# Optimization experiments

Hardware: AMD Instinct MI355X
Metric: run time of the kernel (lower is better)

## Reference

```python
import jax, jax.numpy as jnp
import numpy as np

N_HEAD, BS, F_IN, F_OUT = 4, 8192, 64, 64
LEAKY_ALPHA = 0.2


def setup_inputs() -> dict:
    key = jax.random.key(0)
    k1, k2, k3, k4 = jax.random.split(key, 4)
    return {
        "h": jax.random.normal(k1, (BS, F_IN), dtype=jnp.float32),
        "w": jax.random.normal(k2, (N_HEAD, F_IN, F_OUT), dtype=jnp.float32) * (1.0 / np.sqrt(F_IN)),
        "a_src": jax.random.normal(k3, (N_HEAD, F_OUT, 1), dtype=jnp.float32) * (1.0 / np.sqrt(F_OUT)),
        "a_dst": jax.random.normal(k4, (N_HEAD, F_OUT, 1), dtype=jnp.float32) * (1.0 / np.sqrt(F_OUT)),
        "bias": jnp.zeros((F_OUT,), dtype=jnp.float32),
    }


def reference(h, w, a_src, a_dst, bias):
    # h: [bs, f_in] broadcast-matmul with w: [n_head, f_in, f_out] -> [n_head, bs, f_out]
    h_prime = jnp.einsum("bi,hio->hbo", h, w)
    attn_src = jnp.einsum("hbo,ho->hb", h_prime, a_src[..., 0])  # [n_head, bs]
    attn_dst = jnp.einsum("hbo,ho->hb", h_prime, a_dst[..., 0])  # [n_head, bs]
    # additive scores: [n_head, bs, bs]
    attn = attn_src[:, :, None] + attn_dst[:, None, :]
    attn = jnp.where(attn >= 0, attn, LEAKY_ALPHA * attn)  # leaky_relu(0.2)
    attn = jax.nn.softmax(attn, axis=-1)
    # dropout is identity at inference
    out = jnp.einsum("hbn,hno->hbo", attn, h_prime) + bias  # [n_head, bs, f_out]
    out = jnp.transpose(out, (1, 0, 2))  # [bs, n_head, f_out]
    return out.reshape(out.shape[0], -1)  # [bs, n_head*f_out]
```

## Files before the change

kernel.cpp:

```cpp
#include <hip/hip_runtime.h>
#include <stdio.h>

#define H 4
#define B 8192
#define M2 (2 * B)
#define F 64
#define ALPHA 0.2f
#define NB 4096
#define DMIN (-8.0f)
#define DSCALE 256.0f
#define TSZ 16
#define NTL2 (M2 / TSZ)
#define PELD 132

__device__ __forceinline__ int bucket_of(float x)
{
  int b = (int)((x - DMIN) * DSCALE);
  return min(max(b, 0), NB - 1);
}

__global__ __launch_bounds__(256) void k_hprime(
    const float* __restrict__ h, const float* __restrict__ w,
    const float* __restrict__ a_src, const float* __restrict__ a_dst,
    float* __restrict__ hp, float* __restrict__ s, float* __restrict__ d)
{
  int head = blockIdx.y;
  int row0 = blockIdx.x * 64;
  __shared__ float wl[F * F];
  __shared__ float hl[64 * F];
  const float4* wsrc = (const float4*)(w + (size_t)head * F * F);
  const float4* hsrc = (const float4*)(h + (size_t)row0 * F);
  float4* wl4 = (float4*)wl;
  float4* hl4 = (float4*)hl;
  for (int t = threadIdx.x; t < F * F / 4; t += 256) { wl4[t] = wsrc[t]; hl4[t] = hsrc[t]; }
  __syncthreads();
  int o  = threadIdx.x & 63;
  int rb = threadIdx.x >> 6;
  float as = a_src[head * F + o];
  float ad = a_dst[head * F + o];
  float acc[16];
#pragma unroll
  for (int rg = 0; rg < 16; ++rg) acc[rg] = 0.f;
#pragma unroll 4
  for (int i4 = 0; i4 < F / 4; ++i4) {
    float w0 = wl[(4 * i4 + 0) * F + o];
    float w1 = wl[(4 * i4 + 1) * F + o];
    float w2 = wl[(4 * i4 + 2) * F + o];
    float w3 = wl[(4 * i4 + 3) * F + o];
#pragma unroll
    for (int rg = 0; rg < 16; ++rg) {
      float4 h4 = *((const float4*)(hl + (rg * 4 + rb) * F) + i4);
      acc[rg] = fmaf(h4.x, w0, fmaf(h4.y, w1, fmaf(h4.z, w2, fmaf(h4.w, w3, acc[rg]))));
    }
  }
#pragma unroll
  for (int rg = 0; rg < 16; ++rg) {
    int r = row0 + rg * 4 + rb;
    hp[((size_t)head * B + r) * F + o] = acc[rg];
    float vs = acc[rg] * as, vd = acc[rg] * ad;
#pragma unroll
    for (int off = 32; off; off >>= 1) { vs += __shfl_down(vs, off); vd += __shfl_down(vd, off); }
    if (o == 0) {
      s[(size_t)head * B + r] = vs;
      d[(size_t)head * B + r] = vd;
    }
  }
}

__global__ __launch_bounds__(1024) void k_hist_scan(
    const float* __restrict__ s, const float* __restrict__ d,
    int* __restrict__ bstart, int* __restrict__ gcur)
{
  int head = blockIdx.x;
  int tid = threadIdx.x;
  __shared__ int hist[NB];
  __shared__ int wtot[16], woff[16];
#pragma unroll
  for (int t = 0; t < NB / 1024; ++t) hist[tid + t * 1024] = 0;
  __syncthreads();
  const float* sh = s + (size_t)head * B;
  const float* dh = d + (size_t)head * B;
#pragma unroll
  for (int t = 0; t < B / 1024; ++t)
    atomicAdd(&hist[bucket_of(-sh[tid + t * 1024])], 1);
#pragma unroll
  for (int t = 0; t < B / 1024; ++t)
    atomicAdd(&hist[bucket_of(dh[tid + t * 1024])], 1);
  __syncthreads();
  int h0 = hist[4 * tid], h1 = hist[4 * tid + 1], h2 = hist[4 * tid + 2], h3 = hist[4 * tid + 3];
  int sum = h0 + h1 + h2 + h3;
  int lane = tid & 63, wid = tid >> 6;
  int run = sum;
#pragma unroll
  for (int off = 1; off < 64; off <<= 1) {
    int v = __shfl_up(run, off);
    if (lane >= off) run += v;
  }
  if (lane == 63) wtot[wid] = run;
  __syncthreads();
  if (tid < 16) {
    int off = 0;
    for (int j = 0; j < tid; ++j) off += wtot[j];
    woff[tid] = off;
  }
  __syncthreads();
  int excl = woff[wid] + run - sum;
  int base = head * (NB + 1) + 4 * tid;
  int gbase = head * NB + 4 * tid;
  int e0 = excl, e1 = e0 + h0, e2 = e1 + h1, e3 = e2 + h2;
  bstart[base] = e0; bstart[base + 1] = e1; bstart[base + 2] = e2; bstart[base + 3] = e3;
  gcur[gbase] = e0; gcur[gbase + 1] = e1; gcur[gbase + 2] = e2; gcur[gbase + 3] = e3;
  if (tid == 1023) bstart[head * (NB + 1) + NB] = e3 + h3;
}

__global__ __launch_bounds__(512) void k_scatter(
    const float* __restrict__ s, const float* __restrict__ d, int* __restrict__ gcur,
    float* __restrict__ vsort, int* __restrict__ gsort)
{
  int head = blockIdx.y;
  int g = blockIdx.x * 512 + threadIdx.x;
  float v = (g < B) ? -s[(size_t)head * B + g] : d[(size_t)head * B + (g - B)];
  int b = bucket_of(v);
  int pos = atomicAdd(&gcur[head * NB + b], 1);
  vsort[(size_t)head * M2 + pos] = v;
  gsort[(size_t)head * M2 + pos] = g;
}

__global__ __launch_bounds__(256) void k_sort(
    const float* __restrict__ vsort, const int* __restrict__ gsort,
    const int* __restrict__ bstart, float* __restrict__ vs2, int* __restrict__ gs2)
{
  int head = blockIdx.y;
  int b = blockIdx.x * 4 + (threadIdx.x >> 6);
  int lane = threadIdx.x & 63;
  int k0 = bstart[head * (NB + 1) + b];
  int k1 = bstart[head * (NB + 1) + b + 1];
  const float* vh = vsort + (size_t)head * M2;
  const int*   gh = gsort + (size_t)head * M2;
  for (int e = k0 + lane; e < k1; e += 64) {
    float vv = vh[e]; int gv = gh[e];
    int rank = 0;
    for (int k = k0; k < k1; ++k) {
      float v2 = vh[k]; int g2 = gh[k];
      rank += (v2 < vv) || (v2 == vv && g2 < gv);
    }
    vs2[(size_t)head * M2 + k0 + rank] = vv;
    gs2[(size_t)head * M2 + k0 + rank] = gv;
  }
}

__global__ __launch_bounds__(256) void k_peA(
    const float* __restrict__ vs2, const int* __restrict__ gs2,
    const float* __restrict__ hp, float* __restrict__ TS)
{
  int head = blockIdx.y;
  int tile = blockIdx.x * 4 + (threadIdx.x >> 6);
  int o = threadIdx.x & 63;
  int k0 = tile * TSZ;
  const float* vsh = vs2 + (size_t)head * M2;
  const int*   gsh = gs2 + (size_t)head * M2;
  const float* hph = hp + (size_t)head * B * F;
  float vv[TSZ]; int gg[TSZ];
#pragma unroll
  for (int j = 0; j < TSZ; ++j) { vv[j] = vsh[k0 + j]; gg[j] = gsh[k0 + j]; }
  float hv[TSZ], e1[TSZ], e2[TSZ];
#pragma unroll
  for (int j = 0; j < TSZ; ++j)
    hv[j] = (gg[j] >= B) ? hph[(size_t)(gg[j] - B) * F + o] : 0.f;
#pragma unroll
  for (int j = 0; j < TSZ; ++j) {
    e1[j] = (gg[j] >= B) ? expf(vv[j]) : 0.f;
    e2[j] = (gg[j] >= B) ? expf(ALPHA * vv[j]) : 0.f;
  }
  float a1 = 0.f, a2 = 0.f, s1 = 0.f, s2 = 0.f;
#pragma unroll
  for (int j = 0; j < TSZ; ++j) {
    a1 = fmaf(e1[j], hv[j], a1);
    a2 = fmaf(e2[j], hv[j], a2);
    s1 += e1[j]; s2 += e2[j];
  }
  float* row = TS + ((size_t)head * NTL2 + tile) * PELD;
  row[o] = a1; row[64 + o] = a2;
  if (o == 0) { row[128] = s1; row[129] = s2; }
}

__global__ __launch_bounds__(64) void k_peB(
    float* __restrict__ TS, float* __restrict__ totals)
{
  int head = blockIdx.y;
  int c = blockIdx.x;
  int lane = threadIdx.x;
  float* base = TS + (size_t)head * NTL2 * PELD + c;
  int t0 = lane * 16;
  float v[16];
#pragma unroll
  for (int t = 0; t < 16; ++t) v[t] = base[(size_t)(t0 + t) * PELD];
  float sum = 0.f;
#pragma unroll
  for (int t = 0; t < 16; ++t) { sum += v[t]; v[t] = sum; }
  float run = sum;
#pragma unroll
  for (int off = 1; off < 64; off <<= 1) {
    float u = __shfl_up(run, off);
    if (lane >= off) run += u;
  }
  float excl = run - sum;
  if (lane == 63) totals[head * PELD + c] = run;
#pragma unroll
  for (int t = 0; t < 16; ++t)
    base[(size_t)(t0 + t) * PELD] = excl + (t == 0 ? 0.f : v[t - 1]);
}

__global__ __launch_bounds__(256) void k_peC_out(
    const float* __restrict__ vs2, const int* __restrict__ gs2,
    const float* __restrict__ hp, const float* __restrict__ TS,
    const float* __restrict__ totals, const float* __restrict__ bias,
    float* __restrict__ out)
{
  int head = blockIdx.y;
  int tile = blockIdx.x * 4 + (threadIdx.x >> 6);
  int o = threadIdx.x & 63;
  int k0 = tile * TSZ;
  const float* vsh = vs2 + (size_t)head * M2;
  const int*   gsh = gs2 + (size_t)head * M2;
  const float* hph = hp + (size_t)head * B * F;
  float vv[TSZ]; int gg[TSZ];
#pragma unroll
  for (int j = 0; j < TSZ; ++j) { vv[j] = vsh[k0 + j]; gg[j] = gsh[k0 + j]; }
  float hv[TSZ], e1[TSZ], e2[TSZ];
#pragma unroll
  for (int j = 0; j < TSZ; ++j)
    hv[j] = (gg[j] >= B) ? hph[(size_t)(gg[j] - B) * F + o] : 0.f;
#pragma unroll
  for (int j = 0; j < TSZ; ++j) {
    e1[j] = (gg[j] >= B) ? expf(vv[j]) : 0.f;
    e2[j] = (gg[j] >= B) ? expf(ALPHA * vv[j]) : 0.f;
  }
  const float* trow = TS + ((size_t)head * NTL2 + tile) * PELD;
  float a1 = trow[o], a2 = trow[64 + o], s1 = trow[128], s2 = trow[129];
  float TE1 = totals[head * PELD + o];
  float T1  = totals[head * PELD + 128];
  float bo  = bias[o];
#pragma unroll
  for (int j = 0; j < TSZ; ++j) {
    if (gg[j] < B) {
      int i = gg[j];
      float si = -vv[j];
      float e1f = expf(si), e2f = expf(ALPHA * si);
      float denom = e2f * s2 + e1f * (T1 - s1);
      float num   = e2f * a2 + e1f * (TE1 - a1);
      out[(size_t)i * (H * F) + head * F + o] = num / denom + bo;
    } else {
      a1 = fmaf(e1[j], hv[j], a1);
      a2 = fmaf(e2[j], hv[j], a2);
      s1 += e1[j]; s2 += e2[j];
    }
  }
}

extern "C" void kernel_launch(void* const* d_in, const int* in_sizes, int n_in,
                              void* d_out, int out_size, void* d_ws, size_t ws_size,
                              hipStream_t stream)
{
  const float* h     = (const float*)d_in[0];
  const float* w     = (const float*)d_in[1];
  const float* a_src = (const float*)d_in[2];
  const float* a_dst = (const float*)d_in[3];
  const float* bias  = (const float*)d_in[4];
  float* out = (float*)d_out;

  float* p = (float*)d_ws;
  float* hp     = p; p += (size_t)H * B * F;
  float* s      = p; p += H * B;
  float* dd     = p; p += H * B;
  float* vsort  = p; p += (size_t)H * M2;
  int*   gsort  = (int*)p; p += (size_t)H * M2;
  float* vs2    = p; p += (size_t)H * M2;
  int*   gs2    = (int*)p; p += (size_t)H * M2;
  float* TS     = p; p += (size_t)H * NTL2 * PELD;
  float* totals = p; p += H * PELD;
  int* bstart   = (int*)p; p += H * (NB + 1);
  int* gcur     = (int*)p; p += H * NB;

  size_t need = (size_t)((char*)p - (char*)d_ws);
  if (ws_size < need) {
    fprintf(stderr, "kernel_launch: ws_size %zu < needed %zu\n", ws_size, need);
    return;
  }

  k_hprime<<<dim3(B / 64, H), 256, 0, stream>>>(h, w, a_src, a_dst, hp, s, dd);
  k_hist_scan<<<H, 1024, 0, stream>>>(s, dd, bstart, gcur);
  k_scatter<<<dim3(M2 / 512, H), 512, 0, stream>>>(s, dd, gcur, vsort, gsort);
  k_sort<<<dim3(NB / 4, H), 256, 0, stream>>>(vsort, gsort, bstart, vs2, gs2);
  k_peA<<<dim3(NTL2 / 4, H), 256, 0, stream>>>(vs2, gs2, hp, TS);
  k_peB<<<dim3(130, H), 64, 0, stream>>>(TS, totals);
  k_peC_out<<<dim3(NTL2 / 4, H), 256, 0, stream>>>(vs2, gs2, hp, TS, totals, bias, out);
}
```

Measured before the change: 75.61 us.

## Split histogram into grid-wide global-atomic kernel and finer-bucket scan

Replaces the single-block-per-head histogram+scan kernel with a grid-parallel histogram using global atomics (zeroed inside k_hprime) followed by a separate scan kernel. The bucket count doubles with finer resolution, so each bucket holds fewer elements for the later per-bucket sort. This removes the serialization of 16K atomics per head in a single block, at the cost of an extra launch, contended global atomics, and twice as many sort blocks.

```diff
diff --git a/kernel.cpp b/kernel.cpp
--- a/kernel.cpp
+++ b/kernel.cpp
@@ -6,9 +6,9 @@
 #define M2 (2 * B)
 #define F 64
 #define ALPHA 0.2f
-#define NB 4096
+#define NB 8192
 #define DMIN (-8.0f)
-#define DSCALE 256.0f
+#define DSCALE 512.0f
 #define TSZ 16
 #define NTL2 (M2 / TSZ)
 #define PELD 132
@@ -22,10 +22,14 @@
 __global__ __launch_bounds__(256) void k_hprime(
     const float* __restrict__ h, const float* __restrict__ w,
     const float* __restrict__ a_src, const float* __restrict__ a_dst,
-    float* __restrict__ hp, float* __restrict__ s, float* __restrict__ d)
+    float* __restrict__ hp, float* __restrict__ s, float* __restrict__ d,
+    int* __restrict__ ghist)
 {
   int head = blockIdx.y;
   int row0 = blockIdx.x * 64;
+  int gt = (blockIdx.y * gridDim.x + blockIdx.x) * 256 + threadIdx.x;
+  if (gt < H * NB) ghist[gt] = 0;
+
   __shared__ float wl[F * F];
   __shared__ float hl[64 * F];
   const float4* wsrc = (const float4*)(w + (size_t)head * F * F);
@@ -67,34 +71,39 @@
   }
 }
 
-__global__ __launch_bounds__(1024) void k_hist_scan(
-    const float* __restrict__ s, const float* __restrict__ d,
-    int* __restrict__ bstart, int* __restrict__ gcur)
+__global__ __launch_bounds__(256) void k_hist(
+    const float* __restrict__ s, const float* __restrict__ d, int* __restrict__ ghist)
+{
+  int head = blockIdx.y;
+  int g = blockIdx.x * 512 + threadIdx.x;
+#pragma unroll
+  for (int t = 0; t < 2; ++t) {
+    int gg = g + t * 256;
+    float v = (gg < B) ? -s[(size_t)head * B + gg]
+                       : d[(size_t)head * B + (gg - B)];
+    atomicAdd(&ghist[head * NB + bucket_of(v)], 1);
+  }
+}
+
+__global__ __launch_bounds__(1024) void k_scan(
+    const int* __restrict__ ghist, int* __restrict__ bstart, int* __restrict__ gcur)
 {
   int head = blockIdx.x;
   int tid = threadIdx.x;
-  __shared__ int hist[NB];
   __shared__ int wtot[16], woff[16];
-#pragma unroll
-  for (int t = 0; t < NB / 1024; ++t) hist[tid + t * 1024] = 0;
-  __syncthreads();
-  const float* sh = s + (size_t)head * B;
-  const float* dh = d + (size_t)head * B;
-#pragma unroll
-  for (int t = 0; t < B / 1024; ++t)
-    atomicAdd(&hist[bucket_of(-sh[tid + t * 1024])], 1);
-#pragma unroll
-  for (int t = 0; t < B / 1024; ++t)
-    atomicAdd(&hist[bucket_of(dh[tid + t * 1024])], 1);
-  __syncthreads();
-  int h0 = hist[4 * tid], h1 = hist[4 * tid + 1], h2 = hist[4 * tid + 2], h3 = hist[4 * tid + 3];
-  int sum = h0 + h1 + h2 + h3;
+  const int* gh = ghist + head * NB + tid * 8;
+  int v[8];
+#pragma unroll
+  for (int t = 0; t < 8; ++t) v[t] = gh[t];
+  int sum = 0;
+#pragma unroll
+  for (int t = 0; t < 8; ++t) { sum += v[t]; v[t] = sum; }
   int lane = tid & 63, wid = tid >> 6;
   int run = sum;
 #pragma unroll
   for (int off = 1; off < 64; off <<= 1) {
-    int v = __shfl_up(run, off);
-    if (lane >= off) run += v;
+    int u = __shfl_up(run, off);
+    if (lane >= off) run += u;
   }
   if (lane == 63) wtot[wid] = run;
   __syncthreads();
@@ -105,12 +114,15 @@
   }
   __syncthreads();
   int excl = woff[wid] + run - sum;
-  int base = head * (NB + 1) + 4 * tid;
-  int gbase = head * NB + 4 * tid;
-  int e0 = excl, e1 = e0 + h0, e2 = e1 + h1, e3 = e2 + h2;
-  bstart[base] = e0; bstart[base + 1] = e1; bstart[base + 2] = e2; bstart[base + 3] = e3;
-  gcur[gbase] = e0; gcur[gbase + 1] = e1; gcur[gbase + 2] = e2; gcur[gbase + 3] = e3;
-  if (tid == 1023) bstart[head * (NB + 1) + NB] = e3 + h3;
+  int bb = head * (NB + 1) + tid * 8;
+  int gb = head * NB + tid * 8;
+#pragma unroll
+  for (int t = 0; t < 8; ++t) {
+    int e = excl + (t == 0 ? 0 : v[t - 1]);
+    bstart[bb + t] = e;
+    gcur[gb + t] = e;
+  }
+  if (tid == 1023) bstart[head * (NB + 1) + NB] = excl + v[7];
 }
 
 __global__ __launch_bounds__(512) void k_scatter(
@@ -279,6 +291,7 @@
   int*   gs2    = (int*)p; p += (size_t)H * M2;
   float* TS     = p; p += (size_t)H * NTL2 * PELD;
   float* totals = p; p += H * PELD;
+  int* ghist    = (int*)p; p += H * NB;
   int* bstart   = (int*)p; p += H * (NB + 1);
   int* gcur     = (int*)p; p += H * NB;
 
@@ -288,8 +301,9 @@
     return;
   }
 
-  k_hprime<<<dim3(B / 64, H), 256, 0, stream>>>(h, w, a_src, a_dst, hp, s, dd);
-  k_hist_scan<<<H, 1024, 0, stream>>>(s, dd, bstart, gcur);
+  k_hprime<<<dim3(B / 64, H), 256, 0, stream>>>(h, w, a_src, a_dst, hp, s, dd, ghist);
+  k_hist<<<dim3(M2 / 512, H), 256, 0, stream>>>(s, dd, ghist);
+  k_scan<<<H, 1024, 0, stream>>>(ghist, bstart, gcur);
   k_scatter<<<dim3(M2 / 512, H), 512, 0, stream>>>(s, dd, gcur, vsort, gsort);
   k_sort<<<dim3(NB / 4, H), 256, 0, stream>>>(vsort, gsort, bstart, vs2, gs2);
   k_peA<<<dim3(NTL2 / 4, H), 256, 0, stream>>>(vs2, gs2, hp, TS);
```

Measured after the change: 86.71 us. 14.7% more time.

## Split histogram into per-partition blocks and separate scan kernel

Applied to the files above, without the earlier changes.

Replaces the single-block-per-head histogram+scan kernel with a 16-partition-per-head histogram kernel writing partial histograms, followed by a scan kernel that sums the partials. This spreads the histogram work over 64 blocks instead of 4, relieving a serial bottleneck on a few CUs. It adds one kernel launch and a global round trip for the partial histograms. The scatter kernel block size also drops from 512 to 256.

```diff
diff --git a/kernel.cpp b/kernel.cpp
--- a/kernel.cpp
+++ b/kernel.cpp
@@ -9,6 +9,7 @@
 #define NB 4096
 #define DMIN (-8.0f)
 #define DSCALE 256.0f
+#define NPART 16
 #define TSZ 16
 #define NTL2 (M2 / TSZ)
 #define PELD 132
@@ -67,34 +68,49 @@
   }
 }
 
-__global__ __launch_bounds__(1024) void k_hist_scan(
-    const float* __restrict__ s, const float* __restrict__ d,
-    int* __restrict__ bstart, int* __restrict__ gcur)
+__global__ __launch_bounds__(256) void k_hist(
+    const float* __restrict__ s, const float* __restrict__ d, int* __restrict__ phist)
+{
+  int head = blockIdx.y, part = blockIdx.x;
+  int tid = threadIdx.x;
+  __shared__ int hist[NB];
+#pragma unroll
+  for (int t = 0; t < NB / 256; ++t) hist[tid + t * 256] = 0;
+  __syncthreads();
+  int g0 = part * (M2 / NPART);
+#pragma unroll
+  for (int t = 0; t < (M2 / NPART) / 256; ++t) {
+    int g = g0 + t * 256 + tid;
+    float v = (g < B) ? -s[(size_t)head * B + g]
+                      : d[(size_t)head * B + (g - B)];
+    atomicAdd(&hist[bucket_of(v)], 1);
+  }
+  __syncthreads();
+  int* ph = phist + ((size_t)head * NPART + part) * NB;
+#pragma unroll
+  for (int t = 0; t < NB / 256; ++t) ph[tid + t * 256] = hist[tid + t * 256];
+}
+
+__global__ __launch_bounds__(1024) void k_scan(
+    const int* __restrict__ phist, int* __restrict__ bstart, int* __restrict__ gcur)
 {
   int head = blockIdx.x;
   int tid = threadIdx.x;
-  __shared__ int hist[NB];
   __shared__ int wtot[16], woff[16];
-#pragma unroll
-  for (int t = 0; t < NB / 1024; ++t) hist[tid + t * 1024] = 0;
-  __syncthreads();
-  const float* sh = s + (size_t)head * B;
-  const float* dh = d + (size_t)head * B;
-#pragma unroll
-  for (int t = 0; t < B / 1024; ++t)
-    atomicAdd(&hist[bucket_of(-sh[tid + t * 1024])], 1);
-#pragma unroll
-  for (int t = 0; t < B / 1024; ++t)
-    atomicAdd(&hist[bucket_of(dh[tid + t * 1024])], 1);
-  __syncthreads();
-  int h0 = hist[4 * tid], h1 = hist[4 * tid + 1], h2 = hist[4 * tid + 2], h3 = hist[4 * tid + 3];
+  int h0 = 0, h1 = 0, h2 = 0, h3 = 0;
+  const int* ph = phist + (size_t)head * NPART * NB + 4 * tid;
+#pragma unroll
+  for (int p = 0; p < NPART; ++p) {
+    h0 += ph[0]; h1 += ph[1]; h2 += ph[2]; h3 += ph[3];
+    ph += NB;
+  }
   int sum = h0 + h1 + h2 + h3;
   int lane = tid & 63, wid = tid >> 6;
   int run = sum;
 #pragma unroll
   for (int off = 1; off < 64; off <<= 1) {
-    int v = __shfl_up(run, off);
-    if (lane >= off) run += v;
+    int u = __shfl_up(run, off);
+    if (lane >= off) run += u;
   }
   if (lane == 63) wtot[wid] = run;
   __syncthreads();
@@ -105,20 +121,20 @@
   }
   __syncthreads();
   int excl = woff[wid] + run - sum;
-  int base = head * (NB + 1) + 4 * tid;
-  int gbase = head * NB + 4 * tid;
+  int bb = head * (NB + 1) + 4 * tid;
+  int gb = head * NB + 4 * tid;
   int e0 = excl, e1 = e0 + h0, e2 = e1 + h1, e3 = e2 + h2;
-  bstart[base] = e0; bstart[base + 1] = e1; bstart[base + 2] = e2; bstart[base + 3] = e3;
-  gcur[gbase] = e0; gcur[gbase + 1] = e1; gcur[gbase + 2] = e2; gcur[gbase + 3] = e3;
+  bstart[bb] = e0; bstart[bb + 1] = e1; bstart[bb + 2] = e2; bstart[bb + 3] = e3;
+  gcur[gb] = e0; gcur[gb + 1] = e1; gcur[gb + 2] = e2; gcur[gb + 3] = e3;
   if (tid == 1023) bstart[head * (NB + 1) + NB] = e3 + h3;
 }
 
-__global__ __launch_bounds__(512) void k_scatter(
+__global__ __launch_bounds__(256) void k_scatter(
     const float* __restrict__ s, const float* __restrict__ d, int* __restrict__ gcur,
     float* __restrict__ vsort, int* __restrict__ gsort)
 {
   int head = blockIdx.y;
-  int g = blockIdx.x * 512 + threadIdx.x;
+  int g = blockIdx.x * 256 + threadIdx.x;
   float v = (g < B) ? -s[(size_t)head * B + g] : d[(size_t)head * B + (g - B)];
   int b = bucket_of(v);
   int pos = atomicAdd(&gcur[head * NB + b], 1);
@@ -279,6 +295,7 @@
   int*   gs2    = (int*)p; p += (size_t)H * M2;
   float* TS     = p; p += (size_t)H * NTL2 * PELD;
   float* totals = p; p += H * PELD;
+  int* phist    = (int*)p; p += (size_t)H * NPART * NB;
   int* bstart   = (int*)p; p += H * (NB + 1);
   int* gcur     = (int*)p; p += H * NB;
 
@@ -289,8 +306,9 @@
   }
 
   k_hprime<<<dim3(B / 64, H), 256, 0, stream>>>(h, w, a_src, a_dst, hp, s, dd);
-  k_hist_scan<<<H, 1024, 0, stream>>>(s, dd, bstart, gcur);
-  k_scatter<<<dim3(M2 / 512, H), 512, 0, stream>>>(s, dd, gcur, vsort, gsort);
+  k_hist<<<dim3(NPART, H), 256, 0, stream>>>(s, dd, phist);
+  k_scan<<<H, 1024, 0, stream>>>(phist, bstart, gcur);
+  k_scatter<<<dim3(M2 / 256, H), 256, 0, stream>>>(s, dd, gcur, vsort, gsort);
   k_sort<<<dim3(NB / 4, H), 256, 0, stream>>>(vsort, gsort, bstart, vs2, gs2);
   k_peA<<<dim3(NTL2 / 4, H), 256, 0, stream>>>(vs2, gs2, hp, TS);
   k_peB<<<dim3(130, H), 64, 0, stream>>>(TS, totals);
```

Measured after the change: 77.03 us. About the same (+1.9%).
